# Optimization experiments

Measured on AMD Instinct MI355X. Metric: run time of the kernel, lower is better.

The kernel has to match this reference:

```python
import jax, jax.numpy as jnp
import numpy as np

T, B, I, H = 512, 64, 256, 256
ACT_EXP2 = 7   # activation scale = 2^-7
W_EXP2 = 8     # weight scale = 2^-8
QMIN, QMAX = -128.0, 127.0  # int8 symmetric, zp=0


def fq(x, exp2_inv):
    """Fake-quantize (round/clamp/dequant) with straight-through estimator."""
    scale = 2.0 ** (-exp2_inv)
    y = jnp.clip(jnp.round(x / scale), QMIN, QMAX) * scale
    return x + jax.lax.stop_gradient(y - x)


def setup_inputs() -> dict:
    key = jax.random.key(0)
    k = jax.random.split(key, 5)
    x = jax.random.normal(k[0], (T, B, I), jnp.float32)
    h0 = jnp.zeros((B, H), jnp.float32)
    W = jax.random.normal(k[1], (I, 3 * H), jnp.float32) / np.sqrt(I)
    R = jax.random.normal(k[2], (H, 3 * H), jnp.float32) / np.sqrt(H)
    bx = jax.random.normal(k[3], (3 * H,), jnp.float32) * 0.1
    br = jax.random.normal(k[4], (3 * H,), jnp.float32) * 0.1
    return {"x": x, "h0": h0, "W": W, "R": R, "bx": bx, "br": br}


def gru_quant(x, h0, W, R, bx, br):
    # quantize weights/biases once (weight.W / weight.R / weight.bx / weight.br)
    Wq = fq(W, W_EXP2)
    Rq = fq(R, W_EXP2)
    bxq = fq(bx, W_EXP2)
    brq = fq(br, W_EXP2)
    # hoisted input matmul: Wx = fq(fq(x) @ Wq)  -> [T, B, 3H]
    Wx = fq(jnp.einsum('tbi,ij->tbj', fq(x, ACT_EXP2), Wq), ACT_EXP2)
    Hh = h0.shape[-1]
    bz, brg, bg = bxq[:Hh], bxq[Hh:2 * Hh], bxq[2 * Hh:]

    def step(h, wx_t):
        hq = fq(h, ACT_EXP2)                      # input.h
        Rh = fq(hq @ Rq, ACT_EXP2)                # matmul.Rh
        v = fq(Rh + brq, ACT_EXP2)                # op.Rh_add_br
        wz, wr, wg = wx_t[:, :Hh], wx_t[:, Hh:2 * Hh], wx_t[:, 2 * Hh:]
        vz, vr, vg = v[:, :Hh], v[:, Hh:2 * Hh], v[:, 2 * Hh:]
        z = fq(jax.nn.sigmoid(fq(wz + bz + vz, ACT_EXP2)), ACT_EXP2)  # gate.z
        r = fq(jax.nn.sigmoid(fq(wr + brg + vr, ACT_EXP2)), ACT_EXP2)  # gate.r
        rRh = fq(r * vg, ACT_EXP2)                # op.rRh
        g = fq(jnp.tanh(fq(wg + bg + rRh, ACT_EXP2)), ACT_EXP2)        # gate.g
        old = fq(z * h, ACT_EXP2)                 # op.old_contrib
        new = fq((1.0 - z) * g, ACT_EXP2)         # op.new_contrib
        h_new = old + new
        return h_new, h_new

    _, hs = jax.lax.scan(step, h0, Wx)  # hs: [T, B, H]
    return hs


def reference(x, h0, W, R, bx, br):
    return gru_quant(x, h0, W, R, bx, br)
```

## Files before the change

kernel.cpp:

```cpp
#include <hip/hip_runtime.h>
#include <hip/hip_bf16.h>
#include <stdint.h>


#define T_STEPS 512
#define BATCH   64
#define IDIM    256
#define HDIM    256
#define N3H     768

typedef int v4i __attribute__((ext_vector_type(4)));

#if defined(__has_builtin)
#if __has_builtin(__builtin_amdgcn_sdot4)
#define DOT4(a,b,c) __builtin_amdgcn_sdot4((int)(a),(int)(b),(int)(c),false)
#endif
#endif
#ifndef DOT4
__device__ __forceinline__ int dot4_sw(uint32_t a, uint32_t b, int c){
  c += (int)(int8_t)(a)      * (int)(int8_t)(b);
  c += (int)(int8_t)(a>>8)   * (int)(int8_t)(b>>8);
  c += (int)(int8_t)(a>>16)  * (int)(int8_t)(b>>16);
  c += (int)(int8_t)(a>>24)  * (int)(int8_t)(b>>24);
  return c;
}
#define DOT4(a,b,c) dot4_sw((uint32_t)(a),(uint32_t)(b),(int)(c))
#endif

__device__ __forceinline__ void barrier_lds() {
  asm volatile("s_waitcnt lgkmcnt(0)\n\ts_barrier" ::: "memory");
}

__device__ __forceinline__ int clamp8(int x)   { return min(127, max(-128, x)); }
__device__ __forceinline__ int rne_half(int y) { int t = y >> 1; return t + (t & y & 1); }
__device__ __forceinline__ int rne_s8(int s)   { return (s + 127 + ((s >> 8) & 1)) >> 8; }
__device__ __forceinline__ int rne_s7(int p)   { return (p + 63 + ((p >> 7) & 1)) >> 7; }

__device__ __forceinline__ int rneclamp(float v) {
  int q = (int)rintf(v);
  return min(127, max(-128, q));
}

__device__ __forceinline__ uint32_t packq4(float4 f, float sc) {
  uint32_t b0 = (uint32_t)(uint8_t)(int8_t)rneclamp(f.x * sc);
  uint32_t b1 = (uint32_t)(uint8_t)(int8_t)rneclamp(f.y * sc);
  uint32_t b2 = (uint32_t)(uint8_t)(int8_t)rneclamp(f.z * sc);
  uint32_t b3 = (uint32_t)(uint8_t)(int8_t)rneclamp(f.w * sc);
  return b0 | (b1 << 8) | (b2 << 16) | (b3 << 24);
}

__global__ void prep_kernel(const float* __restrict__ W, const float* __restrict__ R,
                            const float* __restrict__ bx, const float* __restrict__ br,
                            int8_t* __restrict__ Wq, int8_t* __restrict__ BF,
                            int8_t* __restrict__ bx8, int8_t* __restrict__ br8) {
  const int NW = IDIM * N3H;
  int idx = blockIdx.x * 256 + threadIdx.x;
  if (idx < NW) {
    int k = idx / N3H, j = idx % N3H;
    Wq[((size_t)(k >> 4) * N3H + j) * 16 + (k & 15)] = (int8_t)rneclamp(W[idx] * 256.0f);
  } else if (idx < 2 * NW) {
    int i2 = idx - NW;
    int e = i2 & 15;
    int l = (i2 >> 4) & 63;
    int s = (i2 >> 10) & 3;
    int n = i2 >> 12;
    int k   = s * 64 + ((l >> 4) << 4) + e;
    int col = n * 16 + (l & 15);
    BF[i2] = (int8_t)rneclamp(R[(size_t)k * N3H + col] * 256.0f);
  } else if (idx < 2 * NW + N3H) {
    int i2 = idx - 2 * NW;
    bx8[i2] = (int8_t)rneclamp(bx[i2] * 256.0f);
  } else if (idx < 2 * NW + 2 * N3H) {
    int i2 = idx - 2 * NW - N3H;
    br8[i2] = (int8_t)rneclamp(br[i2] * 256.0f);
  }
}

__global__ __launch_bounds__(768, 1) void gemm_wx_kernel(
    const float* __restrict__ x, const int8_t* __restrict__ Wq,
    int8_t* __restrict__ WxQ8) {
  const int t = blockIdx.x;
  const int j = threadIdx.x;

  __shared__ uint4 xq4[64 * 16];
  uint32_t* xq = (uint32_t*)xq4;

  uint4 w[16];
  const uint4* wp = (const uint4*)Wq;
  #pragma unroll
  for (int kk = 0; kk < 16; ++kk) w[kk] = wp[kk * N3H + j];

  const float4* xg = (const float4*)(x) + (size_t)t * 4096;
  for (int i = j; i < 4096; i += 768) {
    float4 f = xg[i];
    xq[i] = packq4(f, 128.0f);
  }
  __syncthreads();

  for (int r = 0; r < 64; ++r) {
    int s = 0;
    #pragma unroll
    for (int kk = 0; kk < 16; ++kk) {
      uint4 hv = xq4[r * 16 + kk];
      s = DOT4(hv.x, w[kk].x, s);
      s = DOT4(hv.y, w[kk].y, s);
      s = DOT4(hv.z, w[kk].z, s);
      s = DOT4(hv.w, w[kk].w, s);
    }
    int q = clamp8(rne_s8(s));
    WxQ8[((size_t)r * T_STEPS + t) * N3H + j] = (int8_t)q;
  }
}

__global__ __launch_bounds__(512, 1)
void gru_rec14_kernel(
    const float* __restrict__ h0, const int8_t* __restrict__ BF,
    const int8_t* __restrict__ bx8, const int8_t* __restrict__ br8,
    const int8_t* __restrict__ WxQ8, float* __restrict__ out) {
  const int b    = blockIdx.x;
  const int tid  = threadIdx.x;
  const int lane = tid & 63;
  const int wave = tid >> 6;
  const int j    = tid & 255;

  __shared__ alignas(16) int8_t hq[2][256];
  __shared__ int    Sbuf[N3H];
  __shared__ int8_t lutS[256];
  __shared__ int8_t lutT[256];

  v4i bf[6][4];
  {
    const v4i* bp = (const v4i*)BF;
    #pragma unroll
    for (int i = 0; i < 6; ++i)
      #pragma unroll
      for (int s = 0; s < 4; ++s)
        bf[i][s] = bp[((wave * 6 + i) * 4 + s) * 64 + lane];
  }

  int hi = 0, bzc = 0, brc = 0, bgc = 0, vbz = 0, vbr = 0, vbg = 0;
  const int8_t* wxp = WxQ8 + (size_t)b * T_STEPS * N3H + j;
  int wxA0 = 0, wxA1 = 0, wxA2 = 0, wxB0 = 0, wxB1 = 0, wxB2 = 0;
  if (tid < 256) {
    double a = ((double)j - 128.0) / 128.0;
    lutS[j] = (int8_t)min(127, max(-128, (int)rint(128.0 / (1.0 + exp(-a)))));
    lutT[j] = (int8_t)min(127, max(-128, (int)rint(128.0 * tanh(a))));
    bzc = (int)bx8[j];
    brc = (int)bx8[j + 256];
    bgc = (int)bx8[j + 512];
    vbz = (int)br8[j];
    vbr = (int)br8[j + 256];
    vbg = (int)br8[j + 512];
    hi = (int)rintf(h0[b * HDIM + j] * 128.0f);
    hq[0][j] = (int8_t)clamp8(hi);
    wxA0 = (int)wxp[0];   wxA1 = (int)wxp[256];       wxA2 = (int)wxp[512];
    wxB0 = (int)wxp[N3H]; wxB1 = (int)wxp[N3H + 256]; wxB2 = (int)wxp[N3H + 512];
  }
  __syncthreads();

  float* outp = out + (size_t)b * HDIM + j;
  const int kg = (lane >> 4) << 4;

  for (int t = 0; t < T_STEPS; ++t) {
    const int cur = t & 1, nxt = cur ^ 1;

    int nz = 0, nr = 0, ng = 0;
    if (tid < 256) {
      const int8_t* p = wxp + (size_t)min(t + 2, T_STEPS - 1) * N3H;
      nz = (int)p[0]; nr = (int)p[256]; ng = (int)p[512];
    }

    v4i a0 = *(const v4i*)&hq[cur][  0 + kg];
    v4i a1 = *(const v4i*)&hq[cur][ 64 + kg];
    v4i a2 = *(const v4i*)&hq[cur][128 + kg];
    v4i a3 = *(const v4i*)&hq[cur][192 + kg];

    v4i acc[6];
    #pragma unroll
    for (int i = 0; i < 6; ++i) {
      v4i z = {0, 0, 0, 0};
      z = __builtin_amdgcn_mfma_i32_16x16x64_i8(a0, bf[i][0], z, 0, 0, 0);
      z = __builtin_amdgcn_mfma_i32_16x16x64_i8(a1, bf[i][1], z, 0, 0, 0);
      z = __builtin_amdgcn_mfma_i32_16x16x64_i8(a2, bf[i][2], z, 0, 0, 0);
      z = __builtin_amdgcn_mfma_i32_16x16x64_i8(a3, bf[i][3], z, 0, 0, 0);
      acc[i] = z;
    }
    if (lane < 16) {
      #pragma unroll
      for (int i = 0; i < 6; ++i)
        Sbuf[(wave * 6 + i) * 16 + lane] = acc[i][0];
    }
    barrier_lds();

    if (tid < 256) {
      int sz = Sbuf[j], sr = Sbuf[j + 256], sg = Sbuf[j + 512];
      int vz = clamp8(rne_half(2 * clamp8(rne_s8(sz)) + vbz));
      int vr = clamp8(rne_half(2 * clamp8(rne_s8(sr)) + vbr));
      int vg = clamp8(rne_half(2 * clamp8(rne_s8(sg)) + vbg));
      int az = clamp8(rne_half(2 * (wxA0 + vz) + bzc));
      int zi = (int)lutS[az + 128];
      int ar = clamp8(rne_half(2 * (wxA1 + vr) + brc));
      int ri = (int)lutS[ar + 128];
      int rrh = clamp8(rne_s7(ri * vg));
      int ag = clamp8(rne_half(2 * (wxA2 + rrh) + bgc));
      int gi = (int)lutT[ag + 128];
      int oldi = clamp8(rne_s7(zi * hi));
      int newi = clamp8(rne_s7((128 - zi) * gi));
      hi = oldi + newi;
      outp[(size_t)t * BATCH * HDIM] = (float)hi * (1.0f / 128.0f);
      hq[nxt][j] = (int8_t)clamp8(hi);
      wxA0 = wxB0; wxA1 = wxB1; wxA2 = wxB2;
      wxB0 = nz;   wxB1 = nr;   wxB2 = ng;
    }
    barrier_lds();
  }
}

extern "C" void kernel_launch(void* const* d_in, const int* in_sizes, int n_in,
                              void* d_out, int out_size, void* d_ws, size_t ws_size,
                              hipStream_t stream) {
  const float* x  = (const float*)d_in[0];
  const float* h0 = (const float*)d_in[1];
  const float* W  = (const float*)d_in[2];
  const float* R  = (const float*)d_in[3];
  const float* bx = (const float*)d_in[4];
  const float* br = (const float*)d_in[5];
  float* out = (float*)d_out;

  const size_t NW = (size_t)IDIM * N3H;
  int8_t* Wq  = (int8_t*)d_ws;
  int8_t* BF  = Wq + NW;
  int8_t* bx8 = BF + NW;
  int8_t* br8 = bx8 + N3H;
  int8_t* WxQ8 = br8 + N3H;

  {
    int total = (int)(2 * NW + 2 * N3H);
    int blocks = (total + 255) / 256;
    prep_kernel<<<blocks, 256, 0, stream>>>(W, R, bx, br, Wq, BF, bx8, br8);
  }
  gemm_wx_kernel<<<T_STEPS, 768, 0, stream>>>(x, Wq, WxQ8);
  gru_rec14_kernel<<<BATCH, 512, 0, stream>>>(h0, BF, bx8, br8, WxQ8, out);
}
```

Before: 495.4 us.

## Remap MFMA column tiles so gate math stays in registers, drop one barrier

Reassigns the recurrent-weight column tiles so that each wave owns the z, r and g columns for two hidden units. The gate epilogue can then run directly on the MFMA accumulators instead of going through a shared-memory Sbuf exchange. This removes one LDS store/load round trip and one block barrier per timestep. The MFMA chain is also split into two independent accumulators to shorten the dependency chain. In exchange, only 16 lanes per wave do the epilogue, each handling two units serially, so per-thread epilogue work and register use grow.

```diff
diff --git a/kernel.cpp b/kernel.cpp
--- a/kernel.cpp
+++ b/kernel.cpp
@@ -113,7 +113,7 @@
 }
 
 __global__ __launch_bounds__(512, 1)
-void gru_rec14_kernel(
+void gru_rec15_kernel(
     const float* __restrict__ h0, const int8_t* __restrict__ BF,
     const int8_t* __restrict__ bx8, const int8_t* __restrict__ br8,
     const int8_t* __restrict__ WxQ8, float* __restrict__ out) {
@@ -121,10 +121,8 @@
   const int tid  = threadIdx.x;
   const int lane = tid & 63;
   const int wave = tid >> 6;
-  const int j    = tid & 255;
 
   __shared__ alignas(16) int8_t hq[2][256];
-  __shared__ int    Sbuf[N3H];
   __shared__ int8_t lutS[256];
   __shared__ int8_t lutT[256];
 
@@ -132,42 +130,56 @@
   {
     const v4i* bp = (const v4i*)BF;
     #pragma unroll
-    for (int i = 0; i < 6; ++i)
+    for (int i = 0; i < 6; ++i) {
+      int n = wave + (i & 1) * 8 + (i >> 1) * 16;
       #pragma unroll
       for (int s = 0; s < 4; ++s)
-        bf[i][s] = bp[((wave * 6 + i) * 4 + s) * 64 + lane];
-  }
-
-  int hi = 0, bzc = 0, brc = 0, bgc = 0, vbz = 0, vbr = 0, vbg = 0;
-  const int8_t* wxp = WxQ8 + (size_t)b * T_STEPS * N3H + j;
-  int wxA0 = 0, wxA1 = 0, wxA2 = 0, wxB0 = 0, wxB1 = 0, wxB2 = 0;
+        bf[i][s] = bp[(n * 4 + s) * 64 + lane];
+    }
+  }
+
   if (tid < 256) {
-    double a = ((double)j - 128.0) / 128.0;
-    lutS[j] = (int8_t)min(127, max(-128, (int)rint(128.0 / (1.0 + exp(-a)))));
-    lutT[j] = (int8_t)min(127, max(-128, (int)rint(128.0 * tanh(a))));
-    bzc = (int)bx8[j];
-    brc = (int)bx8[j + 256];
-    bgc = (int)bx8[j + 512];
-    vbz = (int)br8[j];
-    vbr = (int)br8[j + 256];
-    vbg = (int)br8[j + 512];
-    hi = (int)rintf(h0[b * HDIM + j] * 128.0f);
-    hq[0][j] = (int8_t)clamp8(hi);
-    wxA0 = (int)wxp[0];   wxA1 = (int)wxp[256];       wxA2 = (int)wxp[512];
-    wxB0 = (int)wxp[N3H]; wxB1 = (int)wxp[N3H + 256]; wxB2 = (int)wxp[N3H + 512];
+    double a = ((double)tid - 128.0) / 128.0;
+    lutS[tid] = (int8_t)min(127, max(-128, (int)rint(128.0 / (1.0 + exp(-a)))));
+    lutT[tid] = (int8_t)min(127, max(-128, (int)rint(128.0 * tanh(a))));
+    int h00 = (int)rintf(h0[b * HDIM + tid] * 128.0f);
+    hq[0][tid] = (int8_t)clamp8(h00);
+  }
+
+  const int col0 = wave * 16 + (lane & 15);
+  const int col1 = col0 + 128;
+  int hi0 = 0, hi1 = 0;
+  int bz0 = 0, br0 = 0, bg0 = 0, vz0b = 0, vr0b = 0, vg0b = 0;
+  int bz1 = 0, br1 = 0, bg1 = 0, vz1b = 0, vr1b = 0, vg1b = 0;
+  const int8_t* wxb = WxQ8 + (size_t)b * T_STEPS * N3H;
+  int z0A = 0, r0A = 0, g0A = 0, z1A = 0, r1A = 0, g1A = 0;
+  int z0B = 0, r0B = 0, g0B = 0, z1B = 0, r1B = 0, g1B = 0;
+  if (lane < 16) {
+    bz0 = (int)bx8[col0]; br0 = (int)bx8[col0 + 256]; bg0 = (int)bx8[col0 + 512];
+    vz0b = (int)br8[col0]; vr0b = (int)br8[col0 + 256]; vg0b = (int)br8[col0 + 512];
+    bz1 = (int)bx8[col1]; br1 = (int)bx8[col1 + 256]; bg1 = (int)bx8[col1 + 512];
+    vz1b = (int)br8[col1]; vr1b = (int)br8[col1 + 256]; vg1b = (int)br8[col1 + 512];
+    hi0 = (int)rintf(h0[b * HDIM + col0] * 128.0f);
+    hi1 = (int)rintf(h0[b * HDIM + col1] * 128.0f);
+    z0A = (int)wxb[col0]; r0A = (int)wxb[col0 + 256]; g0A = (int)wxb[col0 + 512];
+    z1A = (int)wxb[col1]; r1A = (int)wxb[col1 + 256]; g1A = (int)wxb[col1 + 512];
+    z0B = (int)wxb[N3H + col0]; r0B = (int)wxb[N3H + col0 + 256]; g0B = (int)wxb[N3H + col0 + 512];
+    z1B = (int)wxb[N3H + col1]; r1B = (int)wxb[N3H + col1 + 256]; g1B = (int)wxb[N3H + col1 + 512];
   }
   __syncthreads();
 
-  float* outp = out + (size_t)b * HDIM + j;
+  float* outp0 = out + (size_t)b * HDIM + col0;
+  float* outp1 = out + (size_t)b * HDIM + col1;
   const int kg = (lane >> 4) << 4;
 
   for (int t = 0; t < T_STEPS; ++t) {
     const int cur = t & 1, nxt = cur ^ 1;
 
-    int nz = 0, nr = 0, ng = 0;
-    if (tid < 256) {
-      const int8_t* p = wxp + (size_t)min(t + 2, T_STEPS - 1) * N3H;
-      nz = (int)p[0]; nr = (int)p[256]; ng = (int)p[512];
+    int nz0 = 0, nr0 = 0, ng0 = 0, nz1 = 0, nr1 = 0, ng1 = 0;
+    if (lane < 16) {
+      const int8_t* p = wxb + (size_t)min(t + 2, T_STEPS - 1) * N3H;
+      nz0 = (int)p[col0]; nr0 = (int)p[col0 + 256]; ng0 = (int)p[col0 + 512];
+      nz1 = (int)p[col1]; nr1 = (int)p[col1 + 256]; ng1 = (int)p[col1 + 512];
     }
 
     v4i a0 = *(const v4i*)&hq[cur][  0 + kg];
@@ -175,42 +187,56 @@
     v4i a2 = *(const v4i*)&hq[cur][128 + kg];
     v4i a3 = *(const v4i*)&hq[cur][192 + kg];
 
-    v4i acc[6];
+    int s_[6];
     #pragma unroll
     for (int i = 0; i < 6; ++i) {
-      v4i z = {0, 0, 0, 0};
-      z = __builtin_amdgcn_mfma_i32_16x16x64_i8(a0, bf[i][0], z, 0, 0, 0);
-      z = __builtin_amdgcn_mfma_i32_16x16x64_i8(a1, bf[i][1], z, 0, 0, 0);
-      z = __builtin_amdgcn_mfma_i32_16x16x64_i8(a2, bf[i][2], z, 0, 0, 0);
-      z = __builtin_amdgcn_mfma_i32_16x16x64_i8(a3, bf[i][3], z, 0, 0, 0);
-      acc[i] = z;
-    }
+      v4i za = {0, 0, 0, 0}, zb = {0, 0, 0, 0};
+      za = __builtin_amdgcn_mfma_i32_16x16x64_i8(a0, bf[i][0], za, 0, 0, 0);
+      zb = __builtin_amdgcn_mfma_i32_16x16x64_i8(a2, bf[i][2], zb, 0, 0, 0);
+      za = __builtin_amdgcn_mfma_i32_16x16x64_i8(a1, bf[i][1], za, 0, 0, 0);
+      zb = __builtin_amdgcn_mfma_i32_16x16x64_i8(a3, bf[i][3], zb, 0, 0, 0);
+      s_[i] = za[0] + zb[0];
+    }
+
     if (lane < 16) {
-      #pragma unroll
-      for (int i = 0; i < 6; ++i)
-        Sbuf[(wave * 6 + i) * 16 + lane] = acc[i][0];
-    }
-    barrier_lds();
-
-    if (tid < 256) {
-      int sz = Sbuf[j], sr = Sbuf[j + 256], sg = Sbuf[j + 512];
-      int vz = clamp8(rne_half(2 * clamp8(rne_s8(sz)) + vbz));
-      int vr = clamp8(rne_half(2 * clamp8(rne_s8(sr)) + vbr));
-      int vg = clamp8(rne_half(2 * clamp8(rne_s8(sg)) + vbg));
-      int az = clamp8(rne_half(2 * (wxA0 + vz) + bzc));
-      int zi = (int)lutS[az + 128];
-      int ar = clamp8(rne_half(2 * (wxA1 + vr) + brc));
-      int ri = (int)lutS[ar + 128];
-      int rrh = clamp8(rne_s7(ri * vg));
-      int ag = clamp8(rne_half(2 * (wxA2 + rrh) + bgc));
-      int gi = (int)lutT[ag + 128];
-      int oldi = clamp8(rne_s7(zi * hi));
-      int newi = clamp8(rne_s7((128 - zi) * gi));
-      hi = oldi + newi;
-      outp[(size_t)t * BATCH * HDIM] = (float)hi * (1.0f / 128.0f);
-      hq[nxt][j] = (int8_t)clamp8(hi);
-      wxA0 = wxB0; wxA1 = wxB1; wxA2 = wxB2;
-      wxB0 = nz;   wxB1 = nr;   wxB2 = ng;
+      {
+        int vz = clamp8(rne_half(2 * clamp8(rne_s8(s_[0])) + vz0b));
+        int vr = clamp8(rne_half(2 * clamp8(rne_s8(s_[2])) + vr0b));
+        int vg = clamp8(rne_half(2 * clamp8(rne_s8(s_[4])) + vg0b));
+        int az = clamp8(rne_half(2 * (z0A + vz) + bz0));
+        int zi = (int)lutS[az + 128];
+        int ar = clamp8(rne_half(2 * (r0A + vr) + br0));
+        int ri = (int)lutS[ar + 128];
+        int rrh = clamp8(rne_s7(ri * vg));
+        int ag = clamp8(rne_half(2 * (g0A + rrh) + bg0));
+        int gi = (int)lutT[ag + 128];
+        int oldi = clamp8(rne_s7(zi * hi0));
+        int newi = clamp8(rne_s7((128 - zi) * gi));
+        hi0 = oldi + newi;
+        outp0[(size_t)t * BATCH * HDIM] = (float)hi0 * (1.0f / 128.0f);
+        hq[nxt][col0] = (int8_t)clamp8(hi0);
+        z0A = z0B; r0A = r0B; g0A = g0B;
+        z0B = nz0; r0B = nr0; g0B = ng0;
+      }
+      {
+        int vz = clamp8(rne_half(2 * clamp8(rne_s8(s_[1])) + vz1b));
+        int vr = clamp8(rne_half(2 * clamp8(rne_s8(s_[3])) + vr1b));
+        int vg = clamp8(rne_half(2 * clamp8(rne_s8(s_[5])) + vg1b));
+        int az = clamp8(rne_half(2 * (z1A + vz) + bz1));
+        int zi = (int)lutS[az + 128];
+        int ar = clamp8(rne_half(2 * (r1A + vr) + br1));
+        int ri = (int)lutS[ar + 128];
+        int rrh = clamp8(rne_s7(ri * vg));
+        int ag = clamp8(rne_half(2 * (g1A + rrh) + bg1));
+        int gi = (int)lutT[ag + 128];
+        int oldi = clamp8(rne_s7(zi * hi1));
+        int newi = clamp8(rne_s7((128 - zi) * gi));
+        hi1 = oldi + newi;
+        outp1[(size_t)t * BATCH * HDIM] = (float)hi1 * (1.0f / 128.0f);
+        hq[nxt][col1] = (int8_t)clamp8(hi1);
+        z1A = z1B; r1A = r1B; g1A = g1B;
+        z1B = nz1; r1B = nr1; g1B = ng1;
+      }
     }
     barrier_lds();
   }
@@ -240,5 +266,5 @@
     prep_kernel<<<blocks, 256, 0, stream>>>(W, R, bx, br, Wq, BF, bx8, br8);
   }
   gemm_wx_kernel<<<T_STEPS, 768, 0, stream>>>(x, Wq, WxQ8);
-  gru_rec14_kernel<<<BATCH, 512, 0, stream>>>(h0, BF, bx8, br8, WxQ8, out);
-}
+  gru_rec15_kernel<<<BATCH, 512, 0, stream>>>(h0, BF, bx8, br8, WxQ8, out);
+}
```

Result: slower. 600.1 us (+21.2%).
